# Performance work log

Measured on AMD Instinct MI355X. Metric: run time of the kernel, lower is better.

Reference implementation:

```python
import jax, jax.numpy as jnp
import numpy as np

B, T, I, H = 128, 2048, 64, 128


def setup_inputs() -> dict:
    key = jax.random.key(0)
    ks = jax.random.split(key, 7)
    return {
        "input_data": jax.random.normal(ks[0], (B, T, I), dtype=jnp.float32),
        "h0": jax.random.normal(ks[1], (B, H), dtype=jnp.float32),
        "c0": jax.random.normal(ks[2], (B, H), dtype=jnp.float32),
        "W_ih": jax.random.normal(ks[3], (4 * H, I), dtype=jnp.float32) * 0.05,
        "W_hh": jax.random.normal(ks[4], (4 * H, H), dtype=jnp.float32) * 0.05,
        "b_ih": jax.random.normal(ks[5], (4 * H,), dtype=jnp.float32) * 0.05,
        "b_hh": jax.random.normal(ks[6], (4 * H,), dtype=jnp.float32) * 0.05,
    }


def reference(input_data, h0, c0, W_ih, W_hh, b_ih, b_hh):
    # Precompute input projections for all timesteps: [B, T, 4H]
    x_proj = jnp.einsum('bti,gi->btg', input_data, W_ih) + b_ih + b_hh

    def step(carry, xg):
        h, c = carry                      # [B, H]
        gates = xg + h @ W_hh.T           # [B, 4H]
        i_g, f_g, g_g, o_g = jnp.split(gates, 4, axis=-1)  # PyTorch order i,f,g,o
        i_g = jax.nn.sigmoid(i_g)
        f_g = jax.nn.sigmoid(f_g)
        g_g = jnp.tanh(g_g)
        o_g = jax.nn.sigmoid(o_g)
        c_new = f_g * c + i_g * g_g
        h_new = o_g * jnp.tanh(c_new)
        return (h_new, c_new), h_new

    (h_last, c_last), hs = jax.lax.scan(step, (h0, c0), jnp.swapaxes(x_proj, 0, 1))
    input_encoded = jnp.swapaxes(hs, 0, 1)  # [B, T, H]
    return (h_last[None], input_encoded)
```

## Files before the change

kernel.cpp:

```cpp
#include <hip/hip_runtime.h>

#define BB 128
#define TT 2048
#define II 64
#define HH 128
#define GG 512

typedef _Float16 h2 __attribute__((ext_vector_type(2)));

__device__ __forceinline__ h2 mkh2(float a, float b) {
    h2 r; r.x = (_Float16)a; r.y = (_Float16)b; return r;
}

__device__ __forceinline__ h2 u2h(unsigned u) {
    return __builtin_bit_cast(h2, u);
}

__device__ __forceinline__ float fdot2f(h2 a, h2 b, float c) {
#if __has_builtin(__builtin_amdgcn_fdot2)
    return __builtin_amdgcn_fdot2(a, b, c, false);
#else
    return fmaf((float)a.y, (float)b.y, fmaf((float)a.x, (float)b.x, c));
#endif
}

__device__ __forceinline__ float rcp_fast(float x) {
    return __builtin_amdgcn_rcpf(x);
}

__device__ __forceinline__ float tanh_fast(float x) {
    return fmaf(rcp_fast(1.0f + __expf(-2.0f * x)), 2.0f, -1.0f);
}

template <int CTRL>
__device__ __forceinline__ float dppq(float x) {
#if __has_builtin(__builtin_amdgcn_update_dpp)
    int i = __builtin_bit_cast(int, x);
    int r = __builtin_amdgcn_update_dpp(i, i, CTRL, 0xF, 0xF, true);
    return __builtin_bit_cast(float, r);
#else
    return __shfl_xor(x, (CTRL == 177) ? 1 : (CTRL == 78) ? 2 : 3, 4);
#endif
}

__global__ __launch_bounds__(512, 2) void lstm_fused_kernel(
    const float* __restrict__ input,
    const float* __restrict__ h0,
    const float* __restrict__ c0,
    const float* __restrict__ W_ih,
    const float* __restrict__ W_hh,
    const float* __restrict__ b_ih,
    const float* __restrict__ b_hh,
    float* __restrict__ out)
{
    __shared__ __align__(16) h2 s_x[2][II / 2];
    __shared__ __align__(16) h2 s_h[2][HH / 2];

    const int tid  = threadIdx.x;
    const int b    = blockIdx.x;
    const int lane = tid & 63;
    const int w    = tid >> 6;
    const int gt   = lane & 3;
    const int j    = (w << 4) | (lane >> 2);
    const int row  = (gt << 7) | j;

    h2 wih[II / 2];
    h2 whh[HH / 2];
    {
        const float4* p = reinterpret_cast<const float4*>(W_ih + row * II);
#pragma unroll
        for (int q = 0; q < II / 4; ++q) {
            float4 v = p[q];
            wih[2 * q]     = mkh2(v.x, v.y);
            wih[2 * q + 1] = mkh2(v.z, v.w);
        }
    }
    {
        const float4* p = reinterpret_cast<const float4*>(W_hh + row * HH);
#pragma unroll
        for (int q = 0; q < HH / 4; ++q) {
            float4 v = p[q];
            whh[2 * q]     = mkh2(v.x, v.y);
            whh[2 * q + 1] = mkh2(v.z, v.w);
        }
    }
    const float bias = b_ih[row] + b_hh[row];

    float c = c0[(size_t)b * HH + j];
    if (tid < 64) {
        float2 hv = reinterpret_cast<const float2*>(h0 + (size_t)b * HH)[tid];
        s_h[0][tid] = mkh2(hv.x, hv.y);
    }

    const float2* xin = reinterpret_cast<const float2*>(input) + (size_t)b * TT * 32 + tid;
    float2 xb0, xb1, xb2, xb3;
    if (tid < 32) {
        xb0 = xin[(size_t)0 * 32];
        xb1 = xin[(size_t)1 * 32];
        xb2 = xin[(size_t)2 * 32];
        xb3 = xin[(size_t)3 * 32];
        s_x[0][tid] = mkh2(xb0.x, xb0.y);
        xb0 = xin[(size_t)4 * 32];
    }
    __syncthreads();

    float* out_h = out;
    float* out_e = out + BB * HH;
    float hlast = 0.0f;

    auto step = [&](int t, float2& xbn) {
        const int cb = t & 1, nb = cb ^ 1;

        if (tid < 32) {
            s_x[nb][tid] = mkh2(xbn.x, xbn.y);
            int tn = t + 5; if (tn > TT - 1) tn = TT - 1;
            xbn = xin[(size_t)tn * 32];
        }

        const uint4* sx4 = reinterpret_cast<const uint4*>(s_x[cb]);
        const uint4* sh4 = reinterpret_cast<const uint4*>(s_h[cb]);
        float a0 = bias, a1 = 0.0f, a2 = 0.0f, a3 = 0.0f;
#pragma unroll
        for (int q = 0; q < 8; ++q) {
            uint4 v = sx4[q];
            a0 = fdot2f(wih[4 * q + 0], u2h(v.x), a0);
            a1 = fdot2f(wih[4 * q + 1], u2h(v.y), a1);
            a2 = fdot2f(wih[4 * q + 2], u2h(v.z), a2);
            a3 = fdot2f(wih[4 * q + 3], u2h(v.w), a3);
        }
#pragma unroll
        for (int q = 0; q < 16; ++q) {
            uint4 v = sh4[q];
            a0 = fdot2f(whh[4 * q + 0], u2h(v.x), a0);
            a1 = fdot2f(whh[4 * q + 1], u2h(v.y), a1);
            a2 = fdot2f(whh[4 * q + 2], u2h(v.z), a2);
            a3 = fdot2f(whh[4 * q + 3], u2h(v.w), a3);
        }
        float gate = (a0 + a1) + (a2 + a3);

        float pre = (gt == 2) ? 2.0f * gate : gate;
        float sg  = rcp_fast(1.0f + __expf(-pre));
        float act = (gt == 2) ? fmaf(sg, 2.0f, -1.0f) : sg;

        float v0 = act;
        float v1 = dppq<177>(act);
        float v2 = dppq<78>(act);
        float v3 = dppq<27>(act);
        float sA = (gt & 1) ? v1 : v0;
        float sB = (gt & 1) ? v3 : v2;
        float sC = (gt & 1) ? v0 : v1;
        float sD = (gt & 1) ? v2 : v3;
        float iv = (gt & 2) ? sB : sA;
        float gv = (gt & 2) ? sA : sB;
        float fv = (gt & 2) ? sD : sC;
        float ov = (gt & 2) ? sC : sD;

        c = fmaf(fv, c, iv * gv);
        float hv = ov * tanh_fast(c);
        hlast = hv;

        if (gt == 0) reinterpret_cast<_Float16*>(s_h[nb])[j] = (_Float16)hv;
        if (gt == 1) out_e[((size_t)b * TT + t) * HH + j] = hv;

        __syncthreads();
    };

    for (int t0 = 0; t0 < TT; t0 += 4) {
        step(t0 + 0, xb1);
        step(t0 + 1, xb2);
        step(t0 + 2, xb3);
        step(t0 + 3, xb0);
    }

    if (gt == 2) out_h[(size_t)b * HH + j] = hlast;
}

extern "C" void kernel_launch(void* const* d_in, const int* in_sizes, int n_in,
                              void* d_out, int out_size, void* d_ws, size_t ws_size,
                              hipStream_t stream) {
    const float* input = (const float*)d_in[0];
    const float* h0    = (const float*)d_in[1];
    const float* c0    = (const float*)d_in[2];
    const float* W_ih  = (const float*)d_in[3];
    const float* W_hh  = (const float*)d_in[4];
    const float* b_ih  = (const float*)d_in[5];
    const float* b_hh  = (const float*)d_in[6];
    float* out = (float*)d_out;

    hipLaunchKernelGGL(lstm_fused_kernel, dim3(BB), dim3(GG), 0, stream,
                       input, h0, c0, W_ih, W_hh, b_ih, b_hh, out);
}
```

Before: 1.608 ms.

## Split reduction across quad lanes by K instead of by gate

Each quad of lanes now splits the concatenated x/h vector into four K-chunks of 48 and computes all four gates for one hidden unit, instead of each lane owning one full gate row. This cuts LDS reads per lane from 192 to 48 elements and replaces the gate-gather shuffle with a two-stage DPP reduction of four partial sums. In exchange every lane now evaluates all four activations (more transcendental work) and runs four dependent reductions, and x and h are merged into one shared buffer.

```diff
diff --git a/kernel.cpp b/kernel.cpp
--- a/kernel.cpp
+++ b/kernel.cpp
@@ -5,6 +5,8 @@
 #define II 64
 #define HH 128
 #define GG 512
+#define KK 192
+#define KC 48
 
 typedef _Float16 h2 __attribute__((ext_vector_type(2)));
 
@@ -32,6 +34,10 @@
     return fmaf(rcp_fast(1.0f + __expf(-2.0f * x)), 2.0f, -1.0f);
 }
 
+__device__ __forceinline__ float sigmoid_fast(float x) {
+    return rcp_fast(1.0f + __expf(-x));
+}
+
 template <int CTRL>
 __device__ __forceinline__ float dppq(float x) {
 #if __has_builtin(__builtin_amdgcn_update_dpp)
@@ -53,43 +59,35 @@
     const float* __restrict__ b_hh,
     float* __restrict__ out)
 {
-    __shared__ __align__(16) h2 s_x[2][II / 2];
-    __shared__ __align__(16) h2 s_h[2][HH / 2];
+    __shared__ __align__(16) h2 s_xh[2][KK / 2];
 
     const int tid  = threadIdx.x;
     const int b    = blockIdx.x;
     const int lane = tid & 63;
     const int w    = tid >> 6;
-    const int gt   = lane & 3;
+    const int kc   = lane & 3;
     const int j    = (w << 4) | (lane >> 2);
-    const int row  = (gt << 7) | j;
 
-    h2 wih[II / 2];
-    h2 whh[HH / 2];
-    {
-        const float4* p = reinterpret_cast<const float4*>(W_ih + row * II);
+    h2 wreg[4][KC / 2];
+    float bias[4];
 #pragma unroll
-        for (int q = 0; q < II / 4; ++q) {
-            float4 v = p[q];
-            wih[2 * q]     = mkh2(v.x, v.y);
-            wih[2 * q + 1] = mkh2(v.z, v.w);
+    for (int g = 0; g < 4; ++g) {
+        const int row = (g << 7) | j;
+        bias[g] = b_ih[row] + b_hh[row];
+        const float2* wi = reinterpret_cast<const float2*>(W_ih + row * II);
+        const float2* wh = reinterpret_cast<const float2*>(W_hh + row * HH);
+#pragma unroll
+        for (int m = 0; m < KC / 2; ++m) {
+            const int k = KC * kc + 2 * m;
+            float2 v = (k < II) ? wi[k >> 1] : wh[(k - II) >> 1];
+            wreg[g][m] = mkh2(v.x, v.y);
         }
     }
-    {
-        const float4* p = reinterpret_cast<const float4*>(W_hh + row * HH);
-#pragma unroll
-        for (int q = 0; q < HH / 4; ++q) {
-            float4 v = p[q];
-            whh[2 * q]     = mkh2(v.x, v.y);
-            whh[2 * q + 1] = mkh2(v.z, v.w);
-        }
-    }
-    const float bias = b_ih[row] + b_hh[row];
 
     float c = c0[(size_t)b * HH + j];
     if (tid < 64) {
         float2 hv = reinterpret_cast<const float2*>(h0 + (size_t)b * HH)[tid];
-        s_h[0][tid] = mkh2(hv.x, hv.y);
+        s_xh[0][32 + tid] = mkh2(hv.x, hv.y);
     }
 
     const float2* xin = reinterpret_cast<const float2*>(input) + (size_t)b * TT * 32 + tid;
@@ -99,7 +97,7 @@
         xb1 = xin[(size_t)1 * 32];
         xb2 = xin[(size_t)2 * 32];
         xb3 = xin[(size_t)3 * 32];
-        s_x[0][tid] = mkh2(xb0.x, xb0.y);
+        s_xh[0][tid] = mkh2(xb0.x, xb0.y);
         xb0 = xin[(size_t)4 * 32];
     }
     __syncthreads();
@@ -112,55 +110,56 @@
         const int cb = t & 1, nb = cb ^ 1;
 
         if (tid < 32) {
-            s_x[nb][tid] = mkh2(xbn.x, xbn.y);
+            s_xh[nb][tid] = mkh2(xbn.x, xbn.y);
             int tn = t + 5; if (tn > TT - 1) tn = TT - 1;
             xbn = xin[(size_t)tn * 32];
         }
 
-        const uint4* sx4 = reinterpret_cast<const uint4*>(s_x[cb]);
-        const uint4* sh4 = reinterpret_cast<const uint4*>(s_h[cb]);
-        float a0 = bias, a1 = 0.0f, a2 = 0.0f, a3 = 0.0f;
+        const uint4* basep = reinterpret_cast<const uint4*>(
+            reinterpret_cast<const char*>(s_xh[cb]) + kc * (KC * 2));
+
+        float p0 = 0.0f, p1 = 0.0f, p2 = 0.0f, p3 = 0.0f;
 #pragma unroll
-        for (int q = 0; q < 8; ++q) {
-            uint4 v = sx4[q];
-            a0 = fdot2f(wih[4 * q + 0], u2h(v.x), a0);
-            a1 = fdot2f(wih[4 * q + 1], u2h(v.y), a1);
-            a2 = fdot2f(wih[4 * q + 2], u2h(v.z), a2);
-            a3 = fdot2f(wih[4 * q + 3], u2h(v.w), a3);
+        for (int q = 0; q < 6; ++q) {
+            uint4 v = basep[q];
+            p0 = fdot2f(wreg[0][4 * q + 0], u2h(v.x), p0);
+            p1 = fdot2f(wreg[1][4 * q + 0], u2h(v.x), p1);
+            p2 = fdot2f(wreg[2][4 * q + 0], u2h(v.x), p2);
+            p3 = fdot2f(wreg[3][4 * q + 0], u2h(v.x), p3);
+            p0 = fdot2f(wreg[0][4 * q + 1], u2h(v.y), p0);
+            p1 = fdot2f(wreg[1][4 * q + 1], u2h(v.y), p1);
+            p2 = fdot2f(wreg[2][4 * q + 1], u2h(v.y), p2);
+            p3 = fdot2f(wreg[3][4 * q + 1], u2h(v.y), p3);
+            p0 = fdot2f(wreg[0][4 * q + 2], u2h(v.z), p0);
+            p1 = fdot2f(wreg[1][4 * q + 2], u2h(v.z), p1);
+            p2 = fdot2f(wreg[2][4 * q + 2], u2h(v.z), p2);
+            p3 = fdot2f(wreg[3][4 * q + 2], u2h(v.z), p3);
+            p0 = fdot2f(wreg[0][4 * q + 3], u2h(v.w), p0);
+            p1 = fdot2f(wreg[1][4 * q + 3], u2h(v.w), p1);
+            p2 = fdot2f(wreg[2][4 * q + 3], u2h(v.w), p2);
+            p3 = fdot2f(wreg[3][4 * q + 3], u2h(v.w), p3);
         }
-#pragma unroll
-        for (int q = 0; q < 16; ++q) {
-            uint4 v = sh4[q];
-            a0 = fdot2f(whh[4 * q + 0], u2h(v.x), a0);
-            a1 = fdot2f(whh[4 * q + 1], u2h(v.y), a1);
-            a2 = fdot2f(whh[4 * q + 2], u2h(v.z), a2);
-            a3 = fdot2f(whh[4 * q + 3], u2h(v.w), a3);
-        }
-        float gate = (a0 + a1) + (a2 + a3);
 
-        float pre = (gt == 2) ? 2.0f * gate : gate;
-        float sg  = rcp_fast(1.0f + __expf(-pre));
-        float act = (gt == 2) ? fmaf(sg, 2.0f, -1.0f) : sg;
+        float u0 = p0 + dppq<177>(p0);
+        float u1 = p1 + dppq<177>(p1);
+        float u2 = p2 + dppq<177>(p2);
+        float u3 = p3 + dppq<177>(p3);
+        u0 += dppq<78>(u0);
+        u1 += dppq<78>(u1);
+        u2 += dppq<78>(u2);
+        u3 += dppq<78>(u3);
 
-        float v0 = act;
-        float v1 = dppq<177>(act);
-        float v2 = dppq<78>(act);
-        float v3 = dppq<27>(act);
-        float sA = (gt & 1) ? v1 : v0;
-        float sB = (gt & 1) ? v3 : v2;
-        float sC = (gt & 1) ? v0 : v1;
-        float sD = (gt & 1) ? v2 : v3;
-        float iv = (gt & 2) ? sB : sA;
-        float gv = (gt & 2) ? sA : sB;
-        float fv = (gt & 2) ? sD : sC;
-        float ov = (gt & 2) ? sC : sD;
+        float ig = sigmoid_fast(u0 + bias[0]);
+        float fg = sigmoid_fast(u1 + bias[1]);
+        float gg = tanh_fast(u2 + bias[2]);
+        float og = sigmoid_fast(u3 + bias[3]);
 
-        c = fmaf(fv, c, iv * gv);
-        float hv = ov * tanh_fast(c);
+        c = fmaf(fg, c, ig * gg);
+        float hv = og * tanh_fast(c);
         hlast = hv;
 
-        if (gt == 0) reinterpret_cast<_Float16*>(s_h[nb])[j] = (_Float16)hv;
-        if (gt == 1) out_e[((size_t)b * TT + t) * HH + j] = hv;
+        if (kc == 0) reinterpret_cast<_Float16*>(s_xh[nb])[II + j] = (_Float16)hv;
+        if (kc == 1) out_e[((size_t)b * TT + t) * HH + j] = hv;
 
         __syncthreads();
     };
@@ -172,7 +171,7 @@
         step(t0 + 3, xb0);
     }
 
-    if (gt == 2) out_h[(size_t)b * HH + j] = hlast;
+    if (kc == 2) out_h[(size_t)b * HH + j] = hlast;
 }
 
 extern "C" void kernel_launch(void* const* d_in, const int* in_sizes, int n_in,
```

Result: faster. 1.572 ms (-2.2%).
